# Performance work log

Measured on AMD Instinct MI355X. Metric: run time of the kernel, lower is better.

The kernel has to match this reference:

```python
import jax, jax.numpy as jnp
import numpy as np

N, DIN, DOUT = 8192, 2048, 2048


def setup_inputs() -> dict:
    key = jax.random.key(0)
    k1, k2, k3 = jax.random.split(key, 3)
    x = jax.random.normal(k1, (N, DIN), dtype=jnp.float32)
    # quantized params: uint8 kernel, uint16 bias (as produced by model.quantize)
    qkernel = jax.random.randint(k2, (DIN, DOUT), 0, 256, dtype=jnp.int32).astype(jnp.uint8)
    qbias = jax.random.randint(k3, (DOUT,), 0, 65536, dtype=jnp.int32).astype(jnp.uint16)
    scale = jnp.array(0.5, dtype=jnp.float32)
    zero_point = jnp.array(0.5, dtype=jnp.float32)
    return {"x": x, "scale": scale, "zero_point": zero_point,
            "qkernel": qkernel, "qbias": qbias}


def reference(x, scale, zero_point, qkernel, qbias) -> jnp.ndarray:
    # quantize(x, b=8, uint8): clip(round(x/scale) + zero_point, 0, 255)
    qmax = 2 ** 8 - 1
    xq = jnp.clip(jnp.round(x / scale) + zero_point, 0, qmax).astype(jnp.uint8)
    acc = jnp.dot(xq, qkernel, preferred_element_type=jnp.uint16)
    acc = (acc + qbias).astype(jnp.uint32)  # uint16 add wraps, then widen
    # dequantize: (x - zero_point) * scale  -> float32
    return (acc - zero_point) * scale
```

## Files before the change

kernel.cpp:

```cpp
#include <hip/hip_runtime.h>
#include <stdint.h>


#define NROWS 8192
#define DIN   2048
#define DOUT  2048

typedef int v4i __attribute__((ext_vector_type(4)));

__device__ inline void gload16(const uint8_t* g, uint8_t* l) {
  __builtin_amdgcn_global_load_lds(
      (__attribute__((address_space(1))) void*)(g),
      (__attribute__((address_space(3))) void*)(l), 16, 0, 0);
}

__global__ __launch_bounds__(256) void kq(const float* __restrict__ x,
                                          const float* __restrict__ sp,
                                          const float* __restrict__ zpp,
                                          uint8_t* __restrict__ xq,
                                          int* __restrict__ rs128) {
  const int row = blockIdx.x;
  const int t = threadIdx.x;
  const float s = sp[0], z = zpp[0];
  const float4* xr = (const float4*)(x + (size_t)row * DIN);
  float4 a = xr[2 * t], b = xr[2 * t + 1];
  float vv[8] = {a.x, a.y, a.z, a.w, b.x, b.y, b.z, b.w};
  uint32_t lo = 0, hi = 0;
  int sum = 0;
#pragma unroll
  for (int i = 0; i < 8; ++i) {
    float tq = rintf(vv[i] / s) + z;
    tq = fminf(fmaxf(tq, 0.0f), 255.0f);
    uint32_t q = (uint32_t)tq;
    sum += (int)q;
    uint32_t qs = (q ^ 0x80u) & 0xFFu;
    if (i < 4) lo |= qs << (8 * i); else hi |= qs << (8 * (i - 4));
  }
  ((uint2*)(xq + (size_t)row * DIN))[t] = make_uint2(lo, hi);
#pragma unroll
  for (int o = 32; o > 0; o >>= 1) sum += __shfl_down(sum, o);
  __shared__ int ws4[4];
  if ((t & 63) == 0) ws4[t >> 6] = sum;
  __syncthreads();
  if (t == 0) rs128[row] = 128 * (ws4[0] + ws4[1] + ws4[2] + ws4[3]);
}

__global__ void kdet(const int* __restrict__ qk, int* __restrict__ flag) {
  __shared__ int sbad;
  int t = threadIdx.x;
  if (t == 0) sbad = 0;
  __syncthreads();
  int bad = 0;
  for (int i = t; i < 1024; i += 256) {
    int v = qk[i];
    if (v < 0 || v > 255) bad = 1;
  }
  if (bad) sbad = 1;
  __syncthreads();
  if (t == 0) flag[0] = sbad;
}

__global__ __launch_bounds__(256) void kt(const void* __restrict__ qk,
                                          const int* __restrict__ flag,
                                          uint8_t* __restrict__ qkT) {
  __shared__ uint8_t tile[64][68];
  const int n0 = blockIdx.x * 64;
  const int k0 = blockIdx.y * 64;
  const int tx = threadIdx.x & 15;
  const int ty = threadIdx.x >> 4;
  const int u8mode = flag[0];
  if (u8mode) {
    const uint8_t* q8 = (const uint8_t*)qk;
#pragma unroll
    for (int j = 0; j < 4; ++j) {
      int r = j * 16 + ty;
      uint32_t w = *(const uint32_t*)(q8 + (size_t)(k0 + r) * DOUT + n0 + tx * 4);
      tile[r][tx * 4 + 0] = (uint8_t)(w & 255u);
      tile[r][tx * 4 + 1] = (uint8_t)((w >> 8) & 255u);
      tile[r][tx * 4 + 2] = (uint8_t)((w >> 16) & 255u);
      tile[r][tx * 4 + 3] = (uint8_t)((w >> 24) & 255u);
    }
  } else {
    const int* q32 = (const int*)qk;
#pragma unroll
    for (int j = 0; j < 4; ++j) {
      int r = j * 16 + ty;
      int4 w = *(const int4*)(q32 + (size_t)(k0 + r) * DOUT + n0 + tx * 4);
      tile[r][tx * 4 + 0] = (uint8_t)w.x;
      tile[r][tx * 4 + 1] = (uint8_t)w.y;
      tile[r][tx * 4 + 2] = (uint8_t)w.z;
      tile[r][tx * 4 + 3] = (uint8_t)w.w;
    }
  }
  __syncthreads();
#pragma unroll
  for (int j = 0; j < 4; ++j) {
    int r = j * 16 + ty;
    uint32_t b0 = tile[tx * 4 + 0][r] ^ 0x80u;
    uint32_t b1 = tile[tx * 4 + 1][r] ^ 0x80u;
    uint32_t b2 = tile[tx * 4 + 2][r] ^ 0x80u;
    uint32_t b3 = tile[tx * 4 + 3][r] ^ 0x80u;
    *(uint32_t*)(qkT + (size_t)(n0 + r) * DIN + k0 + tx * 4) =
        b0 | (b1 << 8) | (b2 << 16) | (b3 << 24);
  }
}

__device__ inline int sumxor(uint32_t w) {
  return (int)((w & 255u) ^ 128u) + (int)(((w >> 8) & 255u) ^ 128u) +
         (int)(((w >> 16) & 255u) ^ 128u) + (int)(((w >> 24) & 255u) ^ 128u);
}

__global__ __launch_bounds__(256) void kc(const uint8_t* __restrict__ qkT,
                                          const void* __restrict__ qbias,
                                          const int* __restrict__ flag,
                                          int* __restrict__ ccomb) {
  const int wid = threadIdx.x >> 6;
  const int l = threadIdx.x & 63;
  const int n = blockIdx.x * 4 + wid;
  const uint4* p = (const uint4*)(qkT + (size_t)n * DIN);
  uint4 u0 = p[2 * l], u1 = p[2 * l + 1];
  int s = sumxor(u0.x) + sumxor(u0.y) + sumxor(u0.z) + sumxor(u0.w) +
          sumxor(u1.x) + sumxor(u1.y) + sumxor(u1.z) + sumxor(u1.w);
#pragma unroll
  for (int o = 32; o > 0; o >>= 1) s += __shfl_down(s, o);
  if (l == 0) {
    int qb = flag[0] ? (int)((const uint16_t*)qbias)[n] : ((const int*)qbias)[n];
    ccomb[n] = 128 * s + qb;
  }
}

__global__ __launch_bounds__(256) void kg(const uint8_t* __restrict__ A,
                                          const uint8_t* __restrict__ B,
                                          const int* __restrict__ rs128,
                                          const int* __restrict__ ccomb,
                                          const float* __restrict__ sp,
                                          const float* __restrict__ zpp,
                                          float* __restrict__ out) {
  __shared__ __align__(16) uint8_t As[128 * 64];
  __shared__ __align__(16) uint8_t Bs[128 * 64];
  const int m0 = blockIdx.x * 128;
  const int n0 = blockIdx.y * 128;
  const int t = threadIdx.x;
  const int l = t & 63;
  const int wid = t >> 6;
  const int wr = wid >> 1;
  const int wc = wid & 1;

  const int o0 = t * 16, o1 = (t + 256) * 16;
  const int r0 = o0 >> 6, r1 = o1 >> 6;
  const int c0 = (o0 >> 4) & 3, c1 = (o1 >> 4) & 3;
  const int cs0 = c0 ^ ((r0 >> 1) & 3), cs1 = c1 ^ ((r1 >> 1) & 3);
  const uint8_t* ga0 = A + (size_t)(m0 + r0) * DIN + cs0 * 16;
  const uint8_t* ga1 = A + (size_t)(m0 + r1) * DIN + cs1 * 16;
  const uint8_t* gb0 = B + (size_t)(n0 + r0) * DIN + cs0 * 16;
  const uint8_t* gb1 = B + (size_t)(n0 + r1) * DIN + cs1 * 16;

  v4i acc[4][4];
#pragma unroll
  for (int i = 0; i < 4; ++i)
#pragma unroll
    for (int j = 0; j < 4; ++j) acc[i][j] = (v4i){0, 0, 0, 0};

  const int rl = l & 15;
  const int kgp = l >> 4;

  for (int k0 = 0; k0 < DIN; k0 += 64) {
    gload16(ga0 + k0, As + o0);
    gload16(ga1 + k0, As + o1);
    gload16(gb0 + k0, Bs + o0);
    gload16(gb1 + k0, Bs + o1);
    __syncthreads();
    v4i af[4], bf[4];
#pragma unroll
    for (int mi = 0; mi < 4; ++mi) {
      int row = wr * 64 + mi * 16 + rl;
      af[mi] = *(const v4i*)(As + row * 64 + ((kgp ^ ((row >> 1) & 3)) << 4));
    }
#pragma unroll
    for (int nj = 0; nj < 4; ++nj) {
      int nr = wc * 64 + nj * 16 + rl;
      bf[nj] = *(const v4i*)(Bs + nr * 64 + ((kgp ^ ((nr >> 1) & 3)) << 4));
    }
#pragma unroll
    for (int mi = 0; mi < 4; ++mi)
#pragma unroll
      for (int nj = 0; nj < 4; ++nj)
        acc[mi][nj] = __builtin_amdgcn_mfma_i32_16x16x64_i8(af[mi], bf[nj], acc[mi][nj], 0, 0, 0);
    __syncthreads();
  }

  const float s = sp[0], z = zpp[0];
  int cc[4];
#pragma unroll
  for (int nj = 0; nj < 4; ++nj) cc[nj] = ccomb[n0 + wc * 64 + nj * 16 + rl];
#pragma unroll
  for (int mi = 0; mi < 4; ++mi) {
#pragma unroll
    for (int r = 0; r < 4; ++r) {
      int row = m0 + wr * 64 + mi * 16 + (l >> 4) * 4 + r;
      int rs = rs128[row];
#pragma unroll
      for (int nj = 0; nj < 4; ++nj) {
        int col = n0 + wc * 64 + nj * 16 + rl;
        uint32_t v = (uint32_t)(acc[mi][nj][r] + rs + cc[nj]) & 0xFFFFu;
        out[(size_t)row * DOUT + col] = ((float)v - z) * s;
      }
    }
  }
}

extern "C" void kernel_launch(void* const* d_in, const int* in_sizes, int n_in,
                              void* d_out, int out_size, void* d_ws, size_t ws_size,
                              hipStream_t stream) {
  const float* x   = (const float*)d_in[0];
  const float* sp  = (const float*)d_in[1];
  const float* zpp = (const float*)d_in[2];
  const void*  qk  = d_in[3];
  const void*  qb  = d_in[4];
  float* out = (float*)d_out;

  uint8_t* ws = (uint8_t*)d_ws;
  uint8_t* xq  = ws;
  uint8_t* qkT = ws + (16u << 20);
  int* rs128 = (int*)(ws + (20u << 20));
  int* ccomb = (int*)(ws + (20u << 20) + (32u << 10));
  int* flag  = (int*)(ws + (20u << 20) + (40u << 10));

  kdet<<<1, 256, 0, stream>>>((const int*)qk, flag);
  kq<<<NROWS, 256, 0, stream>>>(x, sp, zpp, xq, rs128);
  kt<<<dim3(DOUT / 64, DIN / 64), 256, 0, stream>>>(qk, flag, qkT);
  kc<<<DOUT / 4, 256, 0, stream>>>(qkT, qb, flag, ccomb);
  kg<<<dim3(NROWS / 128, DOUT / 128), 256, 0, stream>>>(xq, qkT, rs128, ccomb, sp, zpp, out);
}
```

Measured before the change: 177.6 us.

## Rebuild int8 GEMM with 256x256 tiles, double-buffered LDS, and fused prep kernels

```diff
diff --git a/kernel.cpp b/kernel.cpp
--- a/kernel.cpp
+++ b/kernel.cpp
@@ -14,29 +14,48 @@
       (__attribute__((address_space(3))) void*)(l), 16, 0, 0);
 }
 
+__device__ inline void wgbar() {
+  __builtin_amdgcn_sched_barrier(0);
+  __builtin_amdgcn_s_barrier();
+  __builtin_amdgcn_sched_barrier(0);
+}
+
+__device__ inline uint32_t q4(float4 v, float s, float z, int& sum) {
+  uint32_t w = 0;
+  float e[4] = {v.x, v.y, v.z, v.w};
+#pragma unroll
+  for (int i = 0; i < 4; ++i) {
+    float tq = rintf(e[i] / s) + z;
+    tq = fminf(fmaxf(tq, 0.0f), 255.0f);
+    uint32_t q = (uint32_t)tq;
+    sum += (int)q;
+    w |= ((q ^ 0x80u) & 0xFFu) << (8 * i);
+  }
+  return w;
+}
+
 __global__ __launch_bounds__(256) void kq(const float* __restrict__ x,
                                           const float* __restrict__ sp,
                                           const float* __restrict__ zpp,
                                           uint8_t* __restrict__ xq,
-                                          int* __restrict__ rs128) {
+                                          int* __restrict__ rs128,
+                                          int* __restrict__ ccomb) {
   const int row = blockIdx.x;
   const int t = threadIdx.x;
+  if (row == 0) {
+#pragma unroll
+    for (int i = 0; i < DOUT / 256; ++i) ccomb[i * 256 + t] = 0;
+  }
   const float s = sp[0], z = zpp[0];
   const float4* xr = (const float4*)(x + (size_t)row * DIN);
-  float4 a = xr[2 * t], b = xr[2 * t + 1];
-  float vv[8] = {a.x, a.y, a.z, a.w, b.x, b.y, b.z, b.w};
-  uint32_t lo = 0, hi = 0;
+  float4 a = xr[t];
+  float4 b = xr[t + 256];
   int sum = 0;
-#pragma unroll
-  for (int i = 0; i < 8; ++i) {
-    float tq = rintf(vv[i] / s) + z;
-    tq = fminf(fmaxf(tq, 0.0f), 255.0f);
-    uint32_t q = (uint32_t)tq;
-    sum += (int)q;
-    uint32_t qs = (q ^ 0x80u) & 0xFFu;
-    if (i < 4) lo |= qs << (8 * i); else hi |= qs << (8 * (i - 4));
-  }
-  ((uint2*)(xq + (size_t)row * DIN))[t] = make_uint2(lo, hi);
+  uint32_t w0 = q4(a, s, z, sum);
+  uint32_t w1 = q4(b, s, z, sum);
+  uint32_t* xw = (uint32_t*)(xq + (size_t)row * DIN);
+  xw[t] = w0;
+  xw[t + 256] = w1;
 #pragma unroll
   for (int o = 32; o > 0; o >>= 1) sum += __shfl_down(sum, o);
   __shared__ int ws4[4];
@@ -45,30 +64,29 @@
   if (t == 0) rs128[row] = 128 * (ws4[0] + ws4[1] + ws4[2] + ws4[3]);
 }
 
-__global__ void kdet(const int* __restrict__ qk, int* __restrict__ flag) {
-  __shared__ int sbad;
-  int t = threadIdx.x;
-  if (t == 0) sbad = 0;
-  __syncthreads();
-  int bad = 0;
-  for (int i = t; i < 1024; i += 256) {
-    int v = qk[i];
-    if (v < 0 || v > 255) bad = 1;
-  }
-  if (bad) sbad = 1;
-  __syncthreads();
-  if (t == 0) flag[0] = sbad;
-}
-
 __global__ __launch_bounds__(256) void kt(const void* __restrict__ qk,
-                                          const int* __restrict__ flag,
-                                          uint8_t* __restrict__ qkT) {
+                                          const void* __restrict__ qbias,
+                                          uint8_t* __restrict__ qkT,
+                                          int* __restrict__ ccomb) {
   __shared__ uint8_t tile[64][68];
+  __shared__ int sflag;
+  const int t = threadIdx.x;
+  if (t == 0) sflag = 0;
+  __syncthreads();
+  {
+    const int* q32 = (const int*)qk;
+    int bad = 0;
+#pragma unroll
+    for (int i = 0; i < 4; ++i) bad |= ((unsigned)q32[t + 256 * i] > 255u);
+    if (bad) sflag = 1;
+  }
+  __syncthreads();
+  const int u8mode = sflag;
+
   const int n0 = blockIdx.x * 64;
   const int k0 = blockIdx.y * 64;
-  const int tx = threadIdx.x & 15;
-  const int ty = threadIdx.x >> 4;
-  const int u8mode = flag[0];
+  const int tx = t & 15;
+  const int ty = t >> 4;
   if (u8mode) {
     const uint8_t* q8 = (const uint8_t*)qk;
 #pragma unroll
@@ -96,97 +114,122 @@
 #pragma unroll
   for (int j = 0; j < 4; ++j) {
     int r = j * 16 + ty;
-    uint32_t b0 = tile[tx * 4 + 0][r] ^ 0x80u;
-    uint32_t b1 = tile[tx * 4 + 1][r] ^ 0x80u;
-    uint32_t b2 = tile[tx * 4 + 2][r] ^ 0x80u;
-    uint32_t b3 = tile[tx * 4 + 3][r] ^ 0x80u;
+    uint32_t b0 = tile[tx * 4 + 0][r];
+    uint32_t b1 = tile[tx * 4 + 1][r];
+    uint32_t b2 = tile[tx * 4 + 2][r];
+    uint32_t b3 = tile[tx * 4 + 3][r];
     *(uint32_t*)(qkT + (size_t)(n0 + r) * DIN + k0 + tx * 4) =
-        b0 | (b1 << 8) | (b2 << 16) | (b3 << 24);
-  }
-}
-
-__device__ inline int sumxor(uint32_t w) {
-  return (int)((w & 255u) ^ 128u) + (int)(((w >> 8) & 255u) ^ 128u) +
-         (int)(((w >> 16) & 255u) ^ 128u) + (int)(((w >> 24) & 255u) ^ 128u);
-}
-
-__global__ __launch_bounds__(256) void kc(const uint8_t* __restrict__ qkT,
-                                          const void* __restrict__ qbias,
-                                          const int* __restrict__ flag,
-                                          int* __restrict__ ccomb) {
-  const int wid = threadIdx.x >> 6;
-  const int l = threadIdx.x & 63;
-  const int n = blockIdx.x * 4 + wid;
-  const uint4* p = (const uint4*)(qkT + (size_t)n * DIN);
-  uint4 u0 = p[2 * l], u1 = p[2 * l + 1];
-  int s = sumxor(u0.x) + sumxor(u0.y) + sumxor(u0.z) + sumxor(u0.w) +
-          sumxor(u1.x) + sumxor(u1.y) + sumxor(u1.z) + sumxor(u1.w);
-#pragma unroll
-  for (int o = 32; o > 0; o >>= 1) s += __shfl_down(s, o);
-  if (l == 0) {
-    int qb = flag[0] ? (int)((const uint16_t*)qbias)[n] : ((const int*)qbias)[n];
-    ccomb[n] = 128 * s + qb;
-  }
-}
-
-__global__ __launch_bounds__(256) void kg(const uint8_t* __restrict__ A,
-                                          const uint8_t* __restrict__ B,
-                                          const int* __restrict__ rs128,
-                                          const int* __restrict__ ccomb,
-                                          const float* __restrict__ sp,
-                                          const float* __restrict__ zpp,
-                                          float* __restrict__ out) {
-  __shared__ __align__(16) uint8_t As[128 * 64];
-  __shared__ __align__(16) uint8_t Bs[128 * 64];
-  const int m0 = blockIdx.x * 128;
-  const int n0 = blockIdx.y * 128;
+        (b0 ^ 0x80u) | ((b1 ^ 0x80u) << 8) | ((b2 ^ 0x80u) << 16) | ((b3 ^ 0x80u) << 24);
+    int part = (int)(b0 + b1 + b2 + b3);
+#pragma unroll
+    for (int m = 1; m < 16; m <<= 1) part += __shfl_xor(part, m);
+    if (tx == 0) atomicAdd(&ccomb[n0 + r], part << 7);
+  }
+  if (blockIdx.y == 0 && t < 64) {
+    int n = n0 + t;
+    int qb = u8mode ? (int)((const uint16_t*)qbias)[n] : ((const int*)qbias)[n];
+    atomicAdd(&ccomb[n], qb);
+  }
+}
+
+__global__ __launch_bounds__(512, 2) void kg(const uint8_t* __restrict__ A,
+                                             const uint8_t* __restrict__ B,
+                                             const int* __restrict__ rs128,
+                                             const int* __restrict__ ccomb,
+                                             const float* __restrict__ sp,
+                                             const float* __restrict__ zpp,
+                                             float* __restrict__ out) {
+  __shared__ __align__(16) uint8_t lds[131072];
   const int t = threadIdx.x;
-  const int l = t & 63;
-  const int wid = t >> 6;
-  const int wr = wid >> 1;
-  const int wc = wid & 1;
-
-  const int o0 = t * 16, o1 = (t + 256) * 16;
-  const int r0 = o0 >> 6, r1 = o1 >> 6;
-  const int c0 = (o0 >> 4) & 3, c1 = (o1 >> 4) & 3;
-  const int cs0 = c0 ^ ((r0 >> 1) & 3), cs1 = c1 ^ ((r1 >> 1) & 3);
-  const uint8_t* ga0 = A + (size_t)(m0 + r0) * DIN + cs0 * 16;
-  const uint8_t* ga1 = A + (size_t)(m0 + r1) * DIN + cs1 * 16;
-  const uint8_t* gb0 = B + (size_t)(n0 + r0) * DIN + cs0 * 16;
-  const uint8_t* gb1 = B + (size_t)(n0 + r1) * DIN + cs1 * 16;
-
-  v4i acc[4][4];
-#pragma unroll
-  for (int i = 0; i < 4; ++i)
+  const int l = t & 63, wid = t >> 6;
+  const int wr = wid >> 2, wc = wid & 3;
+  const int rl = l & 15, kgp = l >> 4;
+
+  const int bid = blockIdx.x;
+  const int swz = (bid & 7) * 32 + (bid >> 3);
+  const int m0 = (swz >> 3) * 256;
+  const int n0 = (swz & 7) * 256;
+
+  const int srow = t >> 2;
+  const int sc = (t & 3) ^ (srow & 3);
+  const uint8_t* gA = A + (size_t)(m0 + srow) * DIN + sc * 16;
+  const uint8_t* gA2 = gA + (size_t)128 * DIN;
+  const uint8_t* gB = B + (size_t)(n0 + srow) * DIN + sc * 16;
+  const uint8_t* gB2 = gB + (size_t)128 * DIN;
+  const int sdst = t * 16;
+
+#define STAGE_A(BUF, KS, KB) do {                                   \
+    uint8_t* d_ = lds + (BUF) * 32768 + (KS) * 16384 + sdst;        \
+    gload16(gA + (KB) + (KS) * 64, d_);                             \
+    gload16(gA2 + (KB) + (KS) * 64, d_ + 8192);                     \
+  } while (0)
+#define STAGE_B(BUF, KS, KB) do {                                   \
+    uint8_t* d_ = lds + 65536 + (BUF) * 32768 + (KS) * 16384 + sdst;\
+    gload16(gB + (KB) + (KS) * 64, d_);                             \
+    gload16(gB2 + (KB) + (KS) * 64, d_ + 8192);                     \
+  } while (0)
+
+  const int aoff0 = (wr * 128 + rl) * 64 + ((kgp ^ (rl & 3)) << 4);
+  const int boff0 = 65536 + (wc * 64 + rl) * 64 + ((kgp ^ (rl & 3)) << 4);
+
+  v4i acc[8][4];
+#pragma unroll
+  for (int i = 0; i < 8; ++i)
 #pragma unroll
     for (int j = 0; j < 4; ++j) acc[i][j] = (v4i){0, 0, 0, 0};
-
-  const int rl = l & 15;
-  const int kgp = l >> 4;
-
-  for (int k0 = 0; k0 < DIN; k0 += 64) {
-    gload16(ga0 + k0, As + o0);
-    gload16(ga1 + k0, As + o1);
-    gload16(gb0 + k0, Bs + o0);
-    gload16(gb1 + k0, Bs + o1);
-    __syncthreads();
-    v4i af[4], bf[4];
-#pragma unroll
-    for (int mi = 0; mi < 4; ++mi) {
-      int row = wr * 64 + mi * 16 + rl;
-      af[mi] = *(const v4i*)(As + row * 64 + ((kgp ^ ((row >> 1) & 3)) << 4));
-    }
-#pragma unroll
-    for (int nj = 0; nj < 4; ++nj) {
-      int nr = wc * 64 + nj * 16 + rl;
-      bf[nj] = *(const v4i*)(Bs + nr * 64 + ((kgp ^ ((nr >> 1) & 3)) << 4));
-    }
-#pragma unroll
-    for (int mi = 0; mi < 4; ++mi)
-#pragma unroll
-      for (int nj = 0; nj < 4; ++nj)
-        acc[mi][nj] = __builtin_amdgcn_mfma_i32_16x16x64_i8(af[mi], bf[nj], acc[mi][nj], 0, 0, 0);
-    __syncthreads();
+  v4i af[4], bf[4];
+
+#define LD_A(MH, KH) do {                                            \
+    const uint8_t* ap_ = lds + cur * 32768 + (KH) * 16384 + aoff0 + (MH) * 4096; \
+    _Pragma("unroll")                                                \
+    for (int q = 0; q < 4; ++q) af[q] = *(const v4i*)(ap_ + q * 1024);\
+  } while (0)
+#define LD_B(KH) do {                                                \
+    const uint8_t* bp_ = lds + cur * 32768 + (KH) * 16384 + boff0;   \
+    _Pragma("unroll")                                                \
+    for (int nj = 0; nj < 4; ++nj) bf[nj] = *(const v4i*)(bp_ + nj * 1024); \
+  } while (0)
+#define DO_MFMA(MH) do {                                             \
+    __builtin_amdgcn_s_setprio(1);                                   \
+    _Pragma("unroll")                                                \
+    for (int q = 0; q < 4; ++q)                                      \
+      _Pragma("unroll")                                              \
+      for (int nj = 0; nj < 4; ++nj)                                 \
+        acc[(MH) * 4 + q][nj] = __builtin_amdgcn_mfma_i32_16x16x64_i8(\
+            af[q], bf[nj], acc[(MH) * 4 + q][nj], 0, 0, 0);          \
+    __builtin_amdgcn_s_setprio(0);                                   \
+  } while (0)
+
+  STAGE_A(0, 0, 0);
+  STAGE_B(0, 0, 0);
+  STAGE_A(0, 1, 0);
+  STAGE_B(0, 1, 0);
+
+  int cur = 0;
+  for (int tt = 0; tt < 16; ++tt) {
+    const int nb = cur ^ 1;
+    const int kn = ((tt + 1) & 15) * 128;
+    asm volatile("s_waitcnt vmcnt(4)" ::: "memory");
+    wgbar();
+    LD_B(0);
+    LD_A(0, 0);
+    STAGE_A(nb, 0, kn);
+    DO_MFMA(0);
+    wgbar();
+    LD_A(1, 0);
+    STAGE_B(nb, 0, kn);
+    DO_MFMA(1);
+    asm volatile("s_waitcnt vmcnt(4)" ::: "memory");
+    wgbar();
+    LD_B(1);
+    LD_A(0, 1);
+    STAGE_A(nb, 1, kn);
+    DO_MFMA(0);
+    wgbar();
+    LD_A(1, 1);
+    STAGE_B(nb, 1, kn);
+    DO_MFMA(1);
+    cur = nb;
   }
 
   const float s = sp[0], z = zpp[0];
@@ -194,10 +237,10 @@
 #pragma unroll
   for (int nj = 0; nj < 4; ++nj) cc[nj] = ccomb[n0 + wc * 64 + nj * 16 + rl];
 #pragma unroll
-  for (int mi = 0; mi < 4; ++mi) {
+  for (int mi = 0; mi < 8; ++mi) {
 #pragma unroll
     for (int r = 0; r < 4; ++r) {
-      int row = m0 + wr * 64 + mi * 16 + (l >> 4) * 4 + r;
+      int row = m0 + wr * 128 + mi * 16 + kgp * 4 + r;
       int rs = rs128[row];
 #pragma unroll
       for (int nj = 0; nj < 4; ++nj) {
@@ -207,6 +250,11 @@
       }
     }
   }
+#undef STAGE_A
+#undef STAGE_B
+#undef LD_A
+#undef LD_B
+#undef DO_MFMA
 }
 
 extern "C" void kernel_launch(void* const* d_in, const int* in_sizes, int n_in,
@@ -224,11 +272,8 @@
   uint8_t* qkT = ws + (16u << 20);
   int* rs128 = (int*)(ws + (20u << 20));
   int* ccomb = (int*)(ws + (20u << 20) + (32u << 10));
-  int* flag  = (int*)(ws + (20u << 20) + (40u << 10));
-
-  kdet<<<1, 256, 0, stream>>>((const int*)qk, flag);
-  kq<<<NROWS, 256, 0, stream>>>(x, sp, zpp, xq, rs128);
-  kt<<<dim3(DOUT / 64, DIN / 64), 256, 0, stream>>>(qk, flag, qkT);
-  kc<<<DOUT / 4, 256, 0, stream>>>(qkT, qb, flag, ccomb);
-  kg<<<dim3(NROWS / 128, DOUT / 128), 256, 0, stream>>>(xq, qkT, rs128, ccomb, sp, zpp, out);
-}
+
+  kq<<<NROWS, 256, 0, stream>>>(x, sp, zpp, xq, rs128, ccomb);
+  kt<<<dim3(DOUT / 64, DIN / 64), 256, 0, stream>>>(qk, qb, qkT, ccomb);
+  kg<<<dim3(256), 512, 0, stream>>>(xq, qkT, rs128, ccomb, sp, zpp, out);
+}
```

After: 164.0 us. -7.6%, faster.
